# Optimization experiments

Hardware: AMD Instinct MI355X
Metric: run time of the kernel (lower is better)

Reference implementation:

```python
import jax, jax.numpy as jnp
import numpy as np

B, L, D = 4, 2048, 768
K, M, CK = 12, 1, 4            # heads, thetas, conv kernel size
H = D // (K * M)               # 64
DIM_MEM = K * H                # 768
DIM_EXPAND = H * 3             # 192
DSH = DIM_EXPAND * 2           # 384 swiglu head dim
DST = K * DSH                  # 4608
DIM_FUSED = DIM_MEM + K + DST  # 5388
THETA_MIN, THETA_MAX = 1e-3, 3.0


def setup_inputs() -> dict:
    key = jax.random.key(0)
    ks = jax.random.split(key, 5)
    x = jax.random.normal(ks[0], (B, L, D), jnp.float32)
    W_in = jax.random.normal(ks[1], (D, DIM_FUSED), jnp.float32) * 0.02
    conv_w = jax.random.normal(ks[2], (CK, DIM_MEM + K), jnp.float32) * 0.2  # depthwise taps
    rms_scale = jnp.ones((H,), jnp.float32)
    # theta_raw init (M==1 branch): inverse-sigmoid of geomspace grid
    grid = np.geomspace(THETA_MIN, THETA_MAX, K).reshape(1, 1, K, 1, 1)
    base = np.tile(grid, (1, 1, 1, H, 1))
    u = np.clip((base - THETA_MIN) / (THETA_MAX - THETA_MIN), 1e-4, 1 - 1e-4)
    theta_raw = jnp.asarray(np.log(u) - np.log(1.0 - u), jnp.float32)
    decay_slopes = jnp.asarray(np.log(np.exp(np.geomspace(1e-3, 0.1, K)) - 1.0), jnp.float32)
    score_scale = jnp.ones((K,), jnp.float32)
    tanh_scale = jnp.ones((K,), jnp.float32)
    W_sw = jax.random.normal(ks[3], (2 * K * H * M, DST), jnp.float32) * 0.02
    W_out = jax.random.normal(ks[4], (K * DIM_EXPAND, D), jnp.float32) * 0.02
    return {"x": x, "W_in": W_in, "conv_w": conv_w, "rms_scale": rms_scale,
            "theta_raw": theta_raw, "decay_slopes": decay_slopes,
            "score_scale": score_scale, "tanh_scale": tanh_scale,
            "W_sw": W_sw, "W_out": W_out}


def reference(x, W_in, conv_w, rms_scale, theta_raw, decay_slopes,
              score_scale, tanh_scale, W_sw, W_out):
    # fused in-projection
    z_fused = jnp.einsum('bld,df->blf', x, W_in)
    z_mem = z_fused[..., :DIM_MEM + K]
    skip_direct = z_fused[..., DIM_MEM + K:]
    # causal depthwise conv (kernel size CK, left pad CK-1)
    zp = jnp.pad(z_mem, ((0, 0), (CK - 1, 0), (0, 0)))
    z_conv = sum(zp[:, j:j + L, :] * conv_w[j] for j in range(CK))
    z_mem = jax.nn.silu(z_conv)
    # memory keys + RMSNorm over H
    k_val = z_mem[..., :DIM_MEM].reshape(B, L, K, H)
    k_val = k_val * jax.lax.rsqrt(jnp.mean(k_val * k_val, axis=-1, keepdims=True) + 1e-6) * rms_scale
    s_raw = z_mem[..., DIM_MEM:]  # (B, L, K)
    # theta (M == 1)
    theta = THETA_MIN + (THETA_MAX - THETA_MIN) * jax.nn.sigmoid(theta_raw)  # (1,1,K,H,1)
    # decay time weights (num_anchor_heads == 0, maxlen == L)
    pos = jnp.arange(L, dtype=jnp.float32)
    slopes = jax.nn.softplus(decay_slopes).reshape(1, 1, K)
    dist = jnp.maximum(jnp.float32(L - 1) - pos, 0.0)
    log_time_weight = -slopes * dist[None, :, None]  # (1, L, K)
    log_p = jnp.clip(score_scale[None, None, :] * s_raw, -10.0, 10.0)
    p_w = jnp.exp(log_p + log_time_weight)  # (B, L, K)
    # characteristic-function encoding
    k5 = k_val[..., None]  # (B, L, K, H, 1)
    phi = jnp.tanh(k5 * tanh_scale.reshape(1, 1, K, 1, 1)) * theta
    kvw = k5 * p_w[..., None, None]
    re = kvw * jnp.cos(phi)
    im = kvw * jnp.sin(phi)
    # fused causal cumulative accumulation
    flat = K * H * M
    stack = jnp.concatenate([p_w, re.reshape(B, L, flat), im.reshape(B, L, flat)], axis=-1)
    cs = jnp.cumsum(stack, axis=1)
    den_acc = cs[..., :K]
    re_acc = cs[..., K:K + flat].reshape(B, L, K, H, M)
    im_acc = cs[..., K + flat:].reshape(B, L, K, H, M)
    inv_den = (1.0 / jnp.maximum(den_acc, 1e-4))[..., None, None]
    summary_flat = jnp.stack([re_acc * inv_den, im_acc * inv_den], axis=-1).reshape(B, L, -1)
    # SwiGLU with skip
    y_spectral = jnp.einsum('bls,sf->blf', summary_flat, W_sw).reshape(B, L, K, DSH)
    y_skip = skip_direct.reshape(B, L, K, DSH)
    y_spec_val, y_spec_gate = jnp.split(y_spectral, 2, axis=-1)
    y_skip_val, y_skip_gate = jnp.split(y_skip, 2, axis=-1)
    y_act = (y_spec_val + y_skip_val) * jax.nn.silu(y_spec_gate + y_skip_gate)
    out = jnp.einsum('blf,fd->bld', y_act.reshape(B, L, -1), W_out)
    return out
```

## Files before the change

### kernel.cpp

```cpp
#include <hip/hip_runtime.h>
#include <hip/hip_bf16.h>

#define B_       4
#define L_       2048
#define D_       768
#define K_       12
#define H_       64
#define CK_      4
#define DIM_MEM_ 768
#define DMK      780
#define NT       (B_*L_)
#define NSUM     1536
#define NACT     2304
#define NCHUNK   16
#define CHLEN    (L_/NCHUNK)
#define PSTRIDE  132

typedef __attribute__((ext_vector_type(8))) short          bf16x8;
typedef __attribute__((ext_vector_type(8))) unsigned short u16x8;
typedef __attribute__((ext_vector_type(4))) float          f32x4;

__device__ __forceinline__ ushort f2bf(float v) {
    __hip_bfloat16 h = __float2bfloat16(v);
    return *reinterpret_cast<ushort*>(&h);
}
__device__ __forceinline__ float tanh_fast(float x) {
    float t = __expf(-2.f * fabsf(x));
    float r = (1.f - t) / (1.f + t);
    return copysignf(r, x);
}

struct PrepJobs {
    const float* W[6];
    ushort*      out[6];
    int ldw[6], Kd[6], colbase[6], remap[6], ntx[6];
    int start[7];
    const float* cast_in;
    ushort*      cast_out;
    int n8;
};

__global__ __launch_bounds__(256)
void prep_all(PrepJobs J)
{
    int blk = blockIdx.x;
    if (blk >= J.start[6]) {
        int i = (blk - J.start[6]) * 256 + threadIdx.x;
        if (i < J.n8) {
            float4 v0 = reinterpret_cast<const float4*>(J.cast_in)[2*i];
            float4 v1 = reinterpret_cast<const float4*>(J.cast_in)[2*i + 1];
            u16x8 o;
            o[0] = f2bf(v0.x); o[1] = f2bf(v0.y); o[2] = f2bf(v0.z); o[3] = f2bf(v0.w);
            o[4] = f2bf(v1.x); o[5] = f2bf(v1.y); o[6] = f2bf(v1.z); o[7] = f2bf(v1.w);
            reinterpret_cast<u16x8*>(J.cast_out)[i] = o;
        }
        return;
    }
    int j = 0;
    while (blk >= J.start[j + 1]) ++j;
    int rel = blk - J.start[j];
    int ntx = J.ntx[j];
    int n0 = (rel % ntx) * 32, k0 = (rel / ntx) * 64;
    const float* W = J.W[j];
    int ldw = J.ldw[j], Kd = J.Kd[j], colbase = J.colbase[j], remap = J.remap[j];
    ushort* out = J.out[j];

    __shared__ float tile[64][33];
    int tx = threadIdx.x & 31, ty = threadIdx.x >> 5;
    int n = n0 + tx;
    int c;
    if (remap) {
        int grp = n >> 5, which = (n >> 4) & 1, nn = (grp << 4) + (n & 15);
        c = colbase + (nn / 192) * 384 + which * 192 + (nn % 192);
    } else {
        c = colbase + n;
    }
    #pragma unroll
    for (int r = 0; r < 8; ++r)
        tile[ty + r*8][tx] = W[(size_t)(k0 + ty + r*8) * ldw + c];
    __syncthreads();
    int nl = threadIdx.x >> 3, kg = threadIdx.x & 7;
    u16x8 o;
    #pragma unroll
    for (int t = 0; t < 8; ++t)
        o[t] = f2bf(tile[kg*8 + t][nl]);
    *reinterpret_cast<u16x8*>(&out[(size_t)(n0 + nl) * Kd + k0 + kg*8]) = o;
}

#define GLOAD16(gp, dp) __builtin_amdgcn_global_load_lds( \
    (__attribute__((address_space(1))) const void*)(gp),  \
    (__attribute__((address_space(3))) void*)(dp), 16, 0, 0)

__device__ __forceinline__ void g13_stage(ushort* dst, const ushort* src, int kd)
{
    #pragma unroll
    for (int s = 0; s < 4; ++s)
        GLOAD16(src + (size_t)(32*s)*kd, dst + 2048*s);
}

__global__ __launch_bounds__(256, 2)
void gemm13_1ph(const ushort* __restrict__ A, const ushort* __restrict__ BT,
                float* __restrict__ C, int Kd, int N, int ldc)
{
    __shared__ ushort lds[32768];
    const int tid  = threadIdx.x;
    const int lane = tid & 63, wave = tid >> 6;
    const int lr = lane & 15, quad = lane >> 4, rx = lr & 7;
    const int wr = (wave >> 1) * 64, wc = (wave & 1) * 64;

    const int nwgx = gridDim.x;
    const int orig = blockIdx.x + blockIdx.y * nwgx;
    const int cpx  = (nwgx * gridDim.y) >> 3;
    const int swz  = (orig & 7) * cpx + (orig >> 3);
    const int m0 = (swz / nwgx) * 128, n0 = (swz % nwgx) * 128;
    const int NKT = Kd >> 6;

    const int sr = tid >> 3;
    const int sc = (tid & 7) ^ (sr & 7);
    const ushort* pA = A  + (size_t)(m0 + sr) * Kd + sc * 8;
    const ushort* pB = BT + (size_t)(n0 + sr) * Kd + sc * 8;

    f32x4 acc[4][4] = {};
    const int ca0 = (quad ^ rx) * 8;
    const int ca1 = ((4 + quad) ^ rx) * 8;

    g13_stage(lds + wave*512,         pA, Kd);
    g13_stage(lds + 16384 + wave*512, pB, Kd);
    asm volatile("s_waitcnt vmcnt(0)" ::: "memory");
    __builtin_amdgcn_s_barrier();

    #pragma unroll 1
    for (int g = 0; g < NKT; ++g) {
        const ushort* Ab = lds + (g & 1) * 8192;
        const ushort* Bb = lds + 16384 + (g & 1) * 8192;

        int nk = (g + 1 < NKT) ? g + 1 : NKT - 1;
        g13_stage(lds + ((g + 1) & 1) * 8192 + wave*512,         pA + nk*64, Kd);
        g13_stage(lds + 16384 + ((g + 1) & 1) * 8192 + wave*512, pB + nk*64, Kd);

        bf16x8 af[4][2], bf[4][2];
        #pragma unroll
        for (int i = 0; i < 4; ++i) {
            const ushort* p = Ab + (wr + i*16 + lr) * 64;
            af[i][0] = *reinterpret_cast<const bf16x8*>(p + ca0);
            af[i][1] = *reinterpret_cast<const bf16x8*>(p + ca1);
        }
        #pragma unroll
        for (int j = 0; j < 4; ++j) {
            const ushort* p = Bb + (wc + j*16 + lr) * 64;
            bf[j][0] = *reinterpret_cast<const bf16x8*>(p + ca0);
            bf[j][1] = *reinterpret_cast<const bf16x8*>(p + ca1);
        }
        __builtin_amdgcn_s_setprio(1);
        #pragma unroll
        for (int ks = 0; ks < 2; ++ks)
            #pragma unroll
            for (int i = 0; i < 4; ++i)
                #pragma unroll
                for (int j = 0; j < 4; ++j)
                    acc[i][j] = __builtin_amdgcn_mfma_f32_16x16x32_bf16(
                                    af[i][ks], bf[j][ks], acc[i][j], 0, 0, 0);
        __builtin_amdgcn_s_setprio(0);

        asm volatile("s_waitcnt vmcnt(0)" ::: "memory");
        __builtin_amdgcn_s_barrier();
    }

    #pragma unroll
    for (int i = 0; i < 4; ++i)
        #pragma unroll
        for (int j = 0; j < 4; ++j)
            #pragma unroll
            for (int r = 0; r < 4; ++r) {
                int row = m0 + wr + i*16 + quad*4 + r;
                int col = n0 + wc + j*16 + lr;
                if (col < N)
                    C[(size_t)row * ldc + col] = acc[i][j][r];
            }
}

#define G2NKT 36

__device__ __forceinline__ void g2_stageA(ushort* lds_, int kt,
                                          const ushort* pAs, const ushort* pAx,
                                          int wave, int part)
{
    int ktc = kt > (G2NKT-1) ? (G2NKT-1) : kt;
    const ushort* g; size_t kd;
    if (ktc < 24) { g = pAs + ktc*64;      kd = 1536; }
    else          { g = pAx + (ktc-24)*64; kd = 768;  }
    g += (size_t)(part * 64) * kd;
    ushort* d = lds_ + (kt & 1) * 8192 + part * 4096 + wave * 512;
    GLOAD16(g,           d);
    GLOAD16(g + 32*kd,   d + 2048);
}

__device__ __forceinline__ void g2_stageB(ushort* lds_, int kt,
                                          const ushort* pBs, const ushort* pBx,
                                          int wave)
{
    int ktc = kt > (G2NKT-1) ? (G2NKT-1) : kt;
    const ushort* g; size_t kd;
    if (ktc < 24) { g = pBs + ktc*64;      kd = 1536; }
    else          { g = pBx + (ktc-24)*64; kd = 768;  }
    ushort* d = lds_ + 16384 + (kt & 1) * 12288 + wave * 512;
    #pragma unroll
    for (int s = 0; s < 6; ++s)
        GLOAD16(g + (size_t)(32*s)*kd, d + 2048*s);
}

__global__ __launch_bounds__(256, 2)
void gemm2_1ph(const ushort* __restrict__ Sm, const ushort* __restrict__ Xb,
               const ushort* __restrict__ WsC, const ushort* __restrict__ WiC,
               ushort* __restrict__ yact)
{
    __shared__ ushort lds[40960];
    const int tid  = threadIdx.x;
    const int lane = tid & 63, wave = tid >> 6;
    const int lr = lane & 15, quad = lane >> 4, rx = lr & 7;
    const int wr = (wave >> 1) * 64;
    const int wc = (wave & 1) * 96;
    const int m0 = blockIdx.y * 128, n0 = blockIdx.x * 192;

    const int sr = tid >> 3;
    const int sc = (tid & 7) ^ (sr & 7);
    const ushort* pAs = Sm  + (size_t)(m0 + sr) * 1536 + sc * 8;
    const ushort* pAx = Xb  + (size_t)(m0 + sr) * 768  + sc * 8;
    const ushort* pBs = WsC + (size_t)(n0 + sr) * 1536 + sc * 8;
    const ushort* pBx = WiC + (size_t)(n0 + sr) * 768  + sc * 8;

    f32x4 acc[4][6] = {};
    const int ca0 = (quad ^ rx) * 8;
    const int ca1 = ((4 + quad) ^ rx) * 8;

    g2_stageA(lds, 0, pAs, pAx, wave, 0);
    g2_stageA(lds, 0, pAs, pAx, wave, 1);
    g2_stageB(lds, 0, pBs, pBx, wave);
    asm volatile("s_waitcnt vmcnt(0)" ::: "memory");
    __builtin_amdgcn_s_barrier();

    #pragma unroll 1
    for (int g = 0; g < G2NKT; ++g) {
        const ushort* Ab = lds + (g & 1) * 8192;
        const ushort* Bb = lds + 16384 + (g & 1) * 12288;

        g2_stageA(lds, g + 1, pAs, pAx, wave, 0);
        g2_stageA(lds, g + 1, pAs, pAx, wave, 1);
        g2_stageB(lds, g + 1, pBs, pBx, wave);

        bf16x8 af[4][2], bfr[6][2];
        #pragma unroll
        for (int i = 0; i < 4; ++i) {
            const ushort* p = Ab + (wr + i*16 + lr) * 64;
            af[i][0] = *reinterpret_cast<const bf16x8*>(p + ca0);
            af[i][1] = *reinterpret_cast<const bf16x8*>(p + ca1);
        }
        #pragma unroll
        for (int j = 0; j < 6; ++j) {
            const ushort* p = Bb + (wc + j*16 + lr) * 64;
            bfr[j][0] = *reinterpret_cast<const bf16x8*>(p + ca0);
            bfr[j][1] = *reinterpret_cast<const bf16x8*>(p + ca1);
        }
        __builtin_amdgcn_s_setprio(1);
        #pragma unroll
        for (int ks = 0; ks < 2; ++ks)
            #pragma unroll
            for (int i = 0; i < 4; ++i)
                #pragma unroll
                for (int j = 0; j < 6; ++j)
                    acc[i][j] = __builtin_amdgcn_mfma_f32_16x16x32_bf16(
                                    af[i][ks], bfr[j][ks], acc[i][j], 0, 0, 0);
        __builtin_amdgcn_s_setprio(0);

        asm volatile("s_waitcnt vmcnt(0)" ::: "memory");
        __builtin_amdgcn_s_barrier();
    }

    const int vg0 = (n0 + wc) >> 5;
    #pragma unroll
    for (int i = 0; i < 4; ++i)
        #pragma unroll
        for (int p = 0; p < 3; ++p)
            #pragma unroll
            for (int r = 0; r < 4; ++r) {
                int row = m0 + wr + i*16 + quad*4 + r;
                int col = (vg0 + p)*16 + lr;
                float v  = acc[i][2*p][r];
                float gt = acc[i][2*p + 1][r];
                float y = v * (gt / (1.f + __expf(-gt)));
                yact[(size_t)row * NACT + col] = f2bf(y);
            }
}

__global__ __launch_bounds__(128)
void token_scan1(const float* __restrict__ zmem, const float* __restrict__ conv_w,
                 const float* __restrict__ rms_scale, const float* __restrict__ theta_raw,
                 const float* __restrict__ dslopes, const float* __restrict__ sscale,
                 const float* __restrict__ tscale,
                 float* __restrict__ reN, float* __restrict__ imN,
                 float* __restrict__ pwN, float* __restrict__ part)
{
    int blk = blockIdx.x;
    int chunk = blk & (NCHUNK - 1);
    int bk = blk >> 4;
    int k = bk % K_;
    int b = bk / K_;
    int tid = threadIdx.x;
    int h = tid & 63;
    int tt = tid >> 6;
    int l0 = chunk * CHLEN + tt * 64;

    int c  = k*H_ + h;
    int cs = DIM_MEM_ + k;

    float cw0 = conv_w[0*DMK + c], cw1 = conv_w[1*DMK + c];
    float cw2 = conv_w[2*DMK + c], cw3 = conv_w[3*DMK + c];
    float cs0 = conv_w[0*DMK + cs], cs1 = conv_w[1*DMK + cs];
    float cs2 = conv_w[2*DMK + cs], cs3 = conv_w[3*DMK + cs];
    float rs  = rms_scale[h];
    float th  = 0.001f + 2.999f * (1.f / (1.f + __expf(-theta_raw[c])));
    float ts  = tscale[k];
    float scl = sscale[k];
    float slope = log1pf(expf(dslopes[k]));

    const float* zb = zmem + (size_t)(b*L_) * DMK;

    float z3=0.f, z2=0.f, z1=0.f, s3=0.f, s2=0.f, s1=0.f;
    {
        int ll = l0 - 3;
        if (ll >= 0)     { z3 = zb[(size_t)ll*DMK + c];     s3 = zb[(size_t)ll*DMK + cs]; }
        if (ll + 1 >= 0) { z2 = zb[(size_t)(ll+1)*DMK + c]; s2 = zb[(size_t)(ll+1)*DMK + cs]; }
        if (ll + 2 >= 0) { z1 = zb[(size_t)(ll+2)*DMK + c]; s1 = zb[(size_t)(ll+2)*DMK + cs]; }
    }

    float sre = 0.f, sim = 0.f, spw = 0.f;
    size_t obase = (size_t)blk * (CHLEN*H_) + (size_t)(tt*64)*H_ + h;

    for (int i0 = 0; i0 < 64; i0 += 8) {
        float zl[8], sl[8];
        #pragma unroll
        for (int j = 0; j < 8; ++j) {
            int l = l0 + i0 + j;
            zl[j] = zb[(size_t)l*DMK + c];
            sl[j] = zb[(size_t)l*DMK + cs];
        }
        #pragma unroll
        for (int j = 0; j < 8; ++j) {
            int l = l0 + i0 + j;
            float a3 = zl[j], b3 = sl[j];
            float acc  = cw0*z3 + cw1*z2 + cw2*z1 + cw3*a3;
            float acc2 = cs0*s3 + cs1*s2 + cs2*s1 + cs3*b3;
            z3 = z2; z2 = z1; z1 = a3;
            s3 = s2; s2 = s1; s1 = b3;

            float kv = acc / (1.f + __expf(-acc));
            float ss = kv * kv;
            #pragma unroll
            for (int off = 32; off > 0; off >>= 1)
                ss += __shfl_xor(ss, off, 64);
            float kn  = kv * rsqrtf(ss * (1.f/64.f) + 1e-6f) * rs;
            float phi = tanh_fast(kn * ts) * th;

            float s  = acc2 / (1.f + expf(-acc2));
            float lp = fminf(10.f, fmaxf(-10.f, scl * s));
            float pwv = expf(lp - slope * (float)(L_ - 1 - l));

            float kvw = kn * pwv;
            float rev = kvw * __cosf(phi);
            float imv = kvw * __sinf(phi);
            reN[obase + (size_t)(i0 + j)*H_] = rev;
            imN[obase + (size_t)(i0 + j)*H_] = imv;
            sre += rev; sim += imv; spw += pwv;
            if (h == 0) pwN[(size_t)bk * L_ + l] = pwv;
        }
    }

    __shared__ float red[2][64], imd[2][64], pwd[2];
    red[tt][h] = sre; imd[tt][h] = sim;
    if (h == 0) pwd[tt] = spw;
    __syncthreads();
    size_t pb = (size_t)blk * PSTRIDE;
    if (tid < 64) part[pb + tid] = red[0][tid] + red[1][tid];
    else          part[pb + tid] = imd[0][tid - 64] + imd[1][tid - 64];
    if (tid == 0) part[pb + 128] = pwd[0] + pwd[1];
}

__global__ __launch_bounds__(128)
void scan_final2(const float* __restrict__ pwN, const float* __restrict__ reN,
                 const float* __restrict__ imN, const float* __restrict__ part,
                 ushort* __restrict__ summary)
{
    int blk = blockIdx.x;
    int chunk = blk & (NCHUNK - 1);
    int bk = blk >> 4;
    int k = bk % K_;
    int b = bk / K_;
    int tid = threadIdx.x;
    int h = tid & 63;
    int pi = tid >> 6;
    const float* __restrict__ src = pi ? imN : reN;
    int l0 = chunk * CHLEN;

    float acc = 0.f, dacc = 0.f;
    size_t pb0 = (size_t)(bk * NCHUNK) * PSTRIDE;
    for (int cn = 0; cn < chunk; ++cn) {
        acc  += part[pb0 + (size_t)cn*PSTRIDE + tid];
        dacc += part[pb0 + (size_t)cn*PSTRIDE + 128];
    }

    size_t base  = (size_t)blk * (CHLEN*H_) + h;
    size_t dbase = (size_t)bk * L_ + l0;
    int outch = 2*(k*H_ + h) + pi;
    for (int i0 = 0; i0 < CHLEN; i0 += 8) {
        float v[8], d[8];
        #pragma unroll
        for (int j = 0; j < 8; ++j) {
            v[j] = src[base + (size_t)(i0 + j)*H_];
            d[j] = pwN[dbase + i0 + j];
        }
        #pragma unroll
        for (int j = 0; j < 8; ++j) {
            acc += v[j]; dacc += d[j];
            float inv = 1.f / fmaxf(dacc, 1e-4f);
            summary[((size_t)(b*L_ + l0 + i0 + j))*NSUM + outch] = f2bf(acc * inv);
        }
    }
}

extern "C" void kernel_launch(void* const* d_in, const int* in_sizes, int n_in,
                              void* d_out, int out_size, void* d_ws, size_t ws_size,
                              hipStream_t stream)
{
    const float* x         = (const float*)d_in[0];
    const float* W_in      = (const float*)d_in[1];
    const float* conv_w    = (const float*)d_in[2];
    const float* rms_scale = (const float*)d_in[3];
    const float* theta_raw = (const float*)d_in[4];
    const float* dslopes   = (const float*)d_in[5];
    const float* sscale    = (const float*)d_in[6];
    const float* tscale    = (const float*)d_in[7];
    const float* W_sw      = (const float*)d_in[8];
    const float* W_out     = (const float*)d_in[9];
    float* out = (float*)d_out;
    char* ws   = (char*)d_ws;

    float*  zmem    = (float*) (ws + 0);
    ushort* summary = (ushort*)(ws + 0);
    float*  pw      = (float*) (ws + 25559040);
    float*  re      = (float*) (ws + 25952256);
    float*  im      = (float*) (ws + 51118080);
    ushort* yact    = (ushort*)(ws + 25952256);
    float*  part    = (float*) (ws + 76283904);
    ushort* xb      = (ushort*)(ws + 76689408);
    ushort* WiCat   = (ushort*)(ws + 89272320);
    ushort* WsCat   = (ushort*)(ws + 96350208);
    ushort* WoT     = (ushort*)(ws + 110505984);
    ushort* WimT    = (ushort*)(ws + 114044928);

    PrepJobs J{};
    J.W[0]=W_in;  J.out[0]=WiCat; J.ldw[0]=5388; J.Kd[0]=768;  J.colbase[0]=780; J.remap[0]=1; J.ntx[0]=144;
    J.W[1]=W_sw;  J.out[1]=WsCat; J.ldw[1]=4608; J.Kd[1]=1536; J.colbase[1]=0;   J.remap[1]=1; J.ntx[1]=144;
    J.W[2]=W_out; J.out[2]=WoT;   J.ldw[2]=768;  J.Kd[2]=2304; J.colbase[2]=0;   J.remap[2]=0; J.ntx[2]=24;
    J.W[3]=W_in;  J.out[3]=WimT;  J.ldw[3]=5388; J.Kd[3]=768;  J.colbase[3]=0;   J.remap[3]=0; J.ntx[3]=28;
    int tiles[4] = {144*12, 144*24, 24*36, 28*12};
    J.start[0] = 0;
    for (int j = 0; j < 4; ++j) J.start[j+1] = J.start[j] + tiles[j];
    J.start[5] = J.start[4];
    J.start[6] = J.start[4];
    J.cast_in = x; J.cast_out = xb; J.n8 = NT*D_/8;
    int nblk = J.start[6] + (J.n8 + 255)/256;

    dim3 blk(256);
    prep_all<<<dim3(nblk), blk, 0, stream>>>(J);
    gemm13_1ph<<<dim3(7, 64), blk, 0, stream>>>(xb, WimT, zmem, 768, 780, 780);
    token_scan1<<<dim3(B_*K_*NCHUNK), dim3(128), 0, stream>>>(
        zmem, conv_w, rms_scale, theta_raw, dslopes, sscale, tscale,
        re, im, pw, part);
    scan_final2<<<dim3(B_*K_*NCHUNK), dim3(128), 0, stream>>>(pw, re, im, part, summary);
    gemm2_1ph<<<dim3(24, 64), dim3(256), 0, stream>>>(summary, xb, WsCat, WiCat, yact);
    gemm13_1ph<<<dim3(6, 64), blk, 0, stream>>>(yact, WoT, out, 2304, 768, 768);
}
```

Before: 377.4 us.

## Recompute scan encoding in emit pass instead of storing intermediate re/im/pw

The first scan pass now only produces per-chunk partial sums, and the emit pass recomputes the conv, SiLU, RMSNorm and characteristic encoding from zmem before writing normalized cumulative summaries. This drops the large re/im/pw round-trip through global memory (about 50 MB written and read back). The cost is doing the transcendental-heavy per-token work twice, and in the emit kernel each of the two half-blocks computes both paths but keeps only one. The workspace layout is repacked so summary no longer aliases zmem.

Result: slower. 436.1 us (+15.6%).

```diff
diff --git a/kernel.cpp b/kernel.cpp
--- a/kernel.cpp
+++ b/kernel.cpp
@@ -293,12 +293,10 @@
 }
 
 __global__ __launch_bounds__(128)
-void token_scan1(const float* __restrict__ zmem, const float* __restrict__ conv_w,
-                 const float* __restrict__ rms_scale, const float* __restrict__ theta_raw,
-                 const float* __restrict__ dslopes, const float* __restrict__ sscale,
-                 const float* __restrict__ tscale,
-                 float* __restrict__ reN, float* __restrict__ imN,
-                 float* __restrict__ pwN, float* __restrict__ part)
+void scan_part(const float* __restrict__ zmem, const float* __restrict__ conv_w,
+               const float* __restrict__ rms_scale, const float* __restrict__ theta_raw,
+               const float* __restrict__ dslopes, const float* __restrict__ sscale,
+               const float* __restrict__ tscale, float* __restrict__ part)
 {
     int blk = blockIdx.x;
     int chunk = blk & (NCHUNK - 1);
@@ -334,7 +332,6 @@
     }
 
     float sre = 0.f, sim = 0.f, spw = 0.f;
-    size_t obase = (size_t)blk * (CHLEN*H_) + (size_t)(tt*64)*H_ + h;
 
     for (int i0 = 0; i0 < 64; i0 += 8) {
         float zl[8], sl[8];
@@ -366,12 +363,9 @@
             float pwv = expf(lp - slope * (float)(L_ - 1 - l));
 
             float kvw = kn * pwv;
-            float rev = kvw * __cosf(phi);
-            float imv = kvw * __sinf(phi);
-            reN[obase + (size_t)(i0 + j)*H_] = rev;
-            imN[obase + (size_t)(i0 + j)*H_] = imv;
-            sre += rev; sim += imv; spw += pwv;
-            if (h == 0) pwN[(size_t)bk * L_ + l] = pwv;
+            sre += kvw * __cosf(phi);
+            sim += kvw * __sinf(phi);
+            spw += pwv;
         }
     }
 
@@ -386,9 +380,11 @@
 }
 
 __global__ __launch_bounds__(128)
-void scan_final2(const float* __restrict__ pwN, const float* __restrict__ reN,
-                 const float* __restrict__ imN, const float* __restrict__ part,
-                 ushort* __restrict__ summary)
+void scan_emit(const float* __restrict__ zmem, const float* __restrict__ conv_w,
+               const float* __restrict__ rms_scale, const float* __restrict__ theta_raw,
+               const float* __restrict__ dslopes, const float* __restrict__ sscale,
+               const float* __restrict__ tscale, const float* __restrict__ part,
+               ushort* __restrict__ summary)
 {
     int blk = blockIdx.x;
     int chunk = blk & (NCHUNK - 1);
@@ -398,7 +394,6 @@
     int tid = threadIdx.x;
     int h = tid & 63;
     int pi = tid >> 6;
-    const float* __restrict__ src = pi ? imN : reN;
     int l0 = chunk * CHLEN;
 
     float acc = 0.f, dacc = 0.f;
@@ -408,21 +403,65 @@
         dacc += part[pb0 + (size_t)cn*PSTRIDE + 128];
     }
 
-    size_t base  = (size_t)blk * (CHLEN*H_) + h;
-    size_t dbase = (size_t)bk * L_ + l0;
+    int c  = k*H_ + h;
+    int cs = DIM_MEM_ + k;
+
+    float cw0 = conv_w[0*DMK + c], cw1 = conv_w[1*DMK + c];
+    float cw2 = conv_w[2*DMK + c], cw3 = conv_w[3*DMK + c];
+    float cs0 = conv_w[0*DMK + cs], cs1 = conv_w[1*DMK + cs];
+    float cs2 = conv_w[2*DMK + cs], cs3 = conv_w[3*DMK + cs];
+    float rs  = rms_scale[h];
+    float th  = 0.001f + 2.999f * (1.f / (1.f + __expf(-theta_raw[c])));
+    float ts  = tscale[k];
+    float scl = sscale[k];
+    float slope = log1pf(expf(dslopes[k]));
+
+    const float* zb = zmem + (size_t)(b*L_) * DMK;
+
+    float z3=0.f, z2=0.f, z1=0.f, s3=0.f, s2=0.f, s1=0.f;
+    {
+        int ll = l0 - 3;
+        if (ll >= 0)     { z3 = zb[(size_t)ll*DMK + c];     s3 = zb[(size_t)ll*DMK + cs]; }
+        if (ll + 1 >= 0) { z2 = zb[(size_t)(ll+1)*DMK + c]; s2 = zb[(size_t)(ll+1)*DMK + cs]; }
+        if (ll + 2 >= 0) { z1 = zb[(size_t)(ll+2)*DMK + c]; s1 = zb[(size_t)(ll+2)*DMK + cs]; }
+    }
+
     int outch = 2*(k*H_ + h) + pi;
+
     for (int i0 = 0; i0 < CHLEN; i0 += 8) {
-        float v[8], d[8];
+        float zl[8], sl[8];
         #pragma unroll
         for (int j = 0; j < 8; ++j) {
-            v[j] = src[base + (size_t)(i0 + j)*H_];
-            d[j] = pwN[dbase + i0 + j];
+            int l = l0 + i0 + j;
+            zl[j] = zb[(size_t)l*DMK + c];
+            sl[j] = zb[(size_t)l*DMK + cs];
         }
         #pragma unroll
         for (int j = 0; j < 8; ++j) {
-            acc += v[j]; dacc += d[j];
+            int l = l0 + i0 + j;
+            float a3 = zl[j], b3 = sl[j];
+            float cacc = cw0*z3 + cw1*z2 + cw2*z1 + cw3*a3;
+            float acc2 = cs0*s3 + cs1*s2 + cs2*s1 + cs3*b3;
+            z3 = z2; z2 = z1; z1 = a3;
+            s3 = s2; s2 = s1; s1 = b3;
+
+            float kv = cacc / (1.f + __expf(-cacc));
+            float ss = kv * kv;
+            #pragma unroll
+            for (int off = 32; off > 0; off >>= 1)
+                ss += __shfl_xor(ss, off, 64);
+            float kn  = kv * rsqrtf(ss * (1.f/64.f) + 1e-6f) * rs;
+            float phi = tanh_fast(kn * ts) * th;
+
+            float s  = acc2 / (1.f + expf(-acc2));
+            float lp = fminf(10.f, fmaxf(-10.f, scl * s));
+            float pwv = expf(lp - slope * (float)(L_ - 1 - l));
+
+            float kvw = kn * pwv;
+            float val = pi ? (kvw * __sinf(phi)) : (kvw * __cosf(phi));
+            acc += val; dacc += pwv;
             float inv = 1.f / fmaxf(dacc, 1e-4f);
-            summary[((size_t)(b*L_ + l0 + i0 + j))*NSUM + outch] = f2bf(acc * inv);
+            summary[((size_t)(b*L_ + l))*NSUM + outch] = f2bf(acc * inv);
         }
     }
 }
@@ -444,18 +483,15 @@
     float* out = (float*)d_out;
     char* ws   = (char*)d_ws;
 
+    ushort* yact    = (ushort*)(ws + 0);
     float*  zmem    = (float*) (ws + 0);
-    ushort* summary = (ushort*)(ws + 0);
-    float*  pw      = (float*) (ws + 25559040);
-    float*  re      = (float*) (ws + 25952256);
-    float*  im      = (float*) (ws + 51118080);
-    ushort* yact    = (ushort*)(ws + 25952256);
-    float*  part    = (float*) (ws + 76283904);
-    ushort* xb      = (ushort*)(ws + 76689408);
-    ushort* WiCat   = (ushort*)(ws + 89272320);
-    ushort* WsCat   = (ushort*)(ws + 96350208);
-    ushort* WoT     = (ushort*)(ws + 110505984);
-    ushort* WimT    = (ushort*)(ws + 114044928);
+    ushort* summary = (ushort*)(ws + 37748736);
+    float*  part    = (float*) (ws + 62914560);
+    ushort* xb      = (ushort*)(ws + 63320064);
+    ushort* WiCat   = (ushort*)(ws + 75902976);
+    ushort* WsCat   = (ushort*)(ws + 82980864);
+    ushort* WoT     = (ushort*)(ws + 97136640);
+    ushort* WimT    = (ushort*)(ws + 100675584);
 
     PrepJobs J{};
     J.W[0]=W_in;  J.out[0]=WiCat; J.ldw[0]=5388; J.Kd[0]=768;  J.colbase[0]=780; J.remap[0]=1; J.ntx[0]=144;
@@ -473,10 +509,10 @@
     dim3 blk(256);
     prep_all<<<dim3(nblk), blk, 0, stream>>>(J);
     gemm13_1ph<<<dim3(7, 64), blk, 0, stream>>>(xb, WimT, zmem, 768, 780, 780);
-    token_scan1<<<dim3(B_*K_*NCHUNK), dim3(128), 0, stream>>>(
-        zmem, conv_w, rms_scale, theta_raw, dslopes, sscale, tscale,
-        re, im, pw, part);
-    scan_final2<<<dim3(B_*K_*NCHUNK), dim3(128), 0, stream>>>(pw, re, im, part, summary);
+    scan_part<<<dim3(B_*K_*NCHUNK), dim3(128), 0, stream>>>(
+        zmem, conv_w, rms_scale, theta_raw, dslopes, sscale, tscale, part);
+    scan_emit<<<dim3(B_*K_*NCHUNK), dim3(128), 0, stream>>>(
+        zmem, conv_w, rms_scale, theta_raw, dslopes, sscale, tscale, part, summary);
     gemm2_1ph<<<dim3(24, 64), dim3(256), 0, stream>>>(summary, xb, WsCat, WiCat, yact);
     gemm13_1ph<<<dim3(6, 64), blk, 0, stream>>>(yact, WoT, out, 2304, 768, 768);
 }
```
